# Optimization experiments

Measured on AMD Instinct MI355X. Metric: run time of the kernel, lower is better.

## Reference

```python
import jax, jax.numpy as jnp
import numpy as np
from jax import lax

B, D, H = 32768, 128, 256
N_ITER = 20


def setup_inputs() -> dict:
    key = jax.random.key(0)
    ks = jax.random.split(key, 7)
    return {
        "r": jax.random.normal(ks[0], (B, D), dtype=jnp.float32),
        "s": jax.random.normal(ks[1], (B, 1), dtype=jnp.float32),
        "pivot": jax.random.normal(ks[2], (D,), dtype=jnp.float32),
        "W1": jax.random.normal(ks[3], (D, H), dtype=jnp.float32) * 0.1,
        "b1": jax.random.normal(ks[4], (H,), dtype=jnp.float32) * 0.1,
        "w2": jax.random.normal(ks[5], (H,), dtype=jnp.float32) * 0.1,
        "b2": jax.random.normal(ks[6], (1,), dtype=jnp.float32) * 0.1,
        "n_iter": N_ITER,
    }


def _omega_step(x, W1, b1, w2, b2):
    # scalar implicit field omega evaluated on [B, D] points -> positive step in (0, 0.1)
    h = jnp.tanh(x @ W1 + b1)                      # [B, H]
    return 0.05 * (1.0 + jnp.tanh(h @ w2 + b2[0]))  # [B]


def reference(r, s, pivot, W1, b1, w2, b2, n_iter):
    # normalize ray directions; norm is detached in the original (stop_gradient)
    norm_of_x = jnp.linalg.norm(r, axis=1, keepdims=True)  # [B, 1]
    r_norm = r / lax.stop_gradient(norm_of_x)              # [B, D]

    # 20-step sphere-tracing-style ray marching along r_norm from pivot
    def step(alpha, _):
        x = pivot[None, :] + alpha[:, None] * r_norm       # [B, D]
        return alpha + _omega_step(x, W1, b1, w2, b2), None

    alpha0 = jnp.zeros((r.shape[0],), dtype=r.dtype)
    res_alpha, _ = lax.scan(step, alpha0, None, length=n_iter)  # [B]

    scale = jax.nn.sigmoid(s) * res_alpha[:, None]         # [B, 1]
    res_x = pivot[None, :] + scale * r_norm                # [B, D]
    return res_x
```

## Files before the change

kernel.cpp:

```cpp
#include <hip/hip_runtime.h>

#define DIM 128
#define HID 256
#define K2LE 2.885390081777927f
#define NTILES 16

typedef __attribute__((ext_vector_type(8))) short bf16x8;
typedef __attribute__((ext_vector_type(4))) float f32x4;

__device__ __forceinline__ unsigned short f2bf(float f) {
    union { float f; unsigned u; } x; x.f = f;
    unsigned r = x.u + 0x7fffu + ((x.u >> 16) & 1u);
    return (unsigned short)(r >> 16);
}
__device__ __forceinline__ float bflo(unsigned u) { return __uint_as_float(u << 16); }
__device__ __forceinline__ float bfhi(unsigned u) { return __uint_as_float(u & 0xffff0000u); }

__device__ __forceinline__ float sigmoid_fast(float x) {
    float t = __builtin_amdgcn_exp2f(-x * 1.4426950408889634f);
    return __builtin_amdgcn_rcpf(1.0f + t);
}

__device__ __forceinline__ float row16_allreduce(float x) {
    int t;
    t = __builtin_amdgcn_update_dpp(0, __float_as_int(x), 0xB1, 0xf, 0xf, true);
    x += __int_as_float(t);
    t = __builtin_amdgcn_update_dpp(0, __float_as_int(x), 0x4E, 0xf, 0xf, true);
    x += __int_as_float(t);
    t = __builtin_amdgcn_update_dpp(0, __float_as_int(x), 0x124, 0xf, 0xf, true);
    x += __int_as_float(t);
    t = __builtin_amdgcn_update_dpp(0, __float_as_int(x), 0x128, 0xf, 0xf, true);
    x += __int_as_float(t);
    return x;
}

__global__ void k_prep(const float* __restrict__ pivot,
                       const float* __restrict__ W1,
                       const float* __restrict__ b1,
                       const float* __restrict__ w2,
                       float* __restrict__ c2p,
                       float* __restrict__ w2p,
                       uint4* __restrict__ W1f) {
    const int tid = threadIdx.x;
    if (blockIdx.x == 0) {
        float a = b1[tid];
#pragma unroll 8
        for (int d = 0; d < DIM; ++d) a = fmaf(pivot[d], W1[d * HID + tid], a);
        const int pidx = (tid & 15) * 16 + (tid >> 4);
        c2p[pidx] = K2LE * a;
        w2p[pidx] = w2[tid];
    }
    const int e  = blockIdx.x * 256 + tid;
    const int m  = e & 15;
    const int q  = (e >> 4) & 3;
    const int kk = (e >> 6) & 3;
    const int nt = e >> 8;
    const int n  = nt * 16 + m;
    const int k0 = kk * 32 + q * 8;
    unsigned w[4];
#pragma unroll
    for (int p = 0; p < 4; ++p) {
        unsigned lo = f2bf(W1[(k0 + 2 * p    ) * HID + n] * K2LE);
        unsigned hi = f2bf(W1[(k0 + 2 * p + 1) * HID + n] * K2LE);
        w[p] = lo | (hi << 16);
    }
    W1f[e] = make_uint4(w[0], w[1], w[2], w[3]);
}

__global__ __launch_bounds__(256, 8) void k_main(
    const float* __restrict__ r,
    const float* __restrict__ s,
    const float* __restrict__ pivot,
    const float* __restrict__ c2p,
    const float* __restrict__ w2p,
    const float* __restrict__ b2,
    const int* __restrict__ n_iter_p,
    const uint4* __restrict__ W1f,
    float* __restrict__ out)
{
    __shared__ unsigned short rnbf[16][128];
    __shared__ float g_x[16][HID];

    const int tid   = threadIdx.x;
    const int lane  = tid & 63;
    const int wave  = tid >> 6;
    const int m     = lane & 15;
    const int q     = lane >> 4;
    const int ray_l = wave * 4 + q;
    const int ray_g = blockIdx.x * 16 + ray_l;
    const int n_iter = *n_iter_p;

    float4 v0 = *(const float4*)&r[ray_g * DIM + m * 8];
    float4 v1 = *(const float4*)&r[ray_g * DIM + m * 8 + 4];
    float ss = v0.x*v0.x + v0.y*v0.y + v0.z*v0.z + v0.w*v0.w
             + v1.x*v1.x + v1.y*v1.y + v1.z*v1.z + v1.w*v1.w;
    ss = row16_allreduce(ss);
    const float inv = __builtin_amdgcn_rsqf(ss);
    unsigned p0 = (unsigned)f2bf(v0.x*inv) | ((unsigned)f2bf(v0.y*inv) << 16);
    unsigned p1 = (unsigned)f2bf(v0.z*inv) | ((unsigned)f2bf(v0.w*inv) << 16);
    unsigned p2 = (unsigned)f2bf(v1.x*inv) | ((unsigned)f2bf(v1.y*inv) << 16);
    unsigned p3 = (unsigned)f2bf(v1.z*inv) | ((unsigned)f2bf(v1.w*inv) << 16);
    *(uint4*)&rnbf[ray_l][m * 8] = make_uint4(p0, p1, p2, p3);
    __syncthreads();

    bf16x8 afrag[4];
#pragma unroll
    for (int kk = 0; kk < 4; ++kk)
        afrag[kk] = *(const bf16x8*)&rnbf[m][kk * 32 + q * 8];

    const bf16x8* __restrict__ wf = (const bf16x8*)W1f;
    const int fb = q * 16 + m;
#pragma unroll
    for (int t = 0; t < 4; ++t) {
        const int nt = wave * 4 + t;
        f32x4 a = {0.f, 0.f, 0.f, 0.f};
#pragma unroll
        for (int kk = 0; kk < 4; ++kk)
            a = __builtin_amdgcn_mfma_f32_16x16x32_bf16(
                    afrag[kk], wf[nt * 256 + kk * 64 + fb], a, 0, 0, 0);
#pragma unroll
        for (int r4 = 0; r4 < 4; ++r4)
            g_x[q * 4 + r4][nt * 16 + m] = a[r4];
    }
    __syncthreads();

    float g[16], c[16], w[16];
#pragma unroll
    for (int i = 0; i < 16; ++i) g[i] = g_x[ray_l][i * 16 + m];
#pragma unroll
    for (int i = 0; i < 4; ++i) {
        float4 cv = *(const float4*)(c2p + m * 16 + i * 4);
        float4 wv = *(const float4*)(w2p + m * 16 + i * 4);
        c[4*i]=cv.x; c[4*i+1]=cv.y; c[4*i+2]=cv.z; c[4*i+3]=cv.w;
        w[4*i]=wv.x; w[4*i+1]=wv.y; w[4*i+2]=wv.z; w[4*i+3]=wv.w;
    }
    float S = 0.f;
#pragma unroll
    for (int i = 0; i < 16; ++i) S += w[i];
    S = row16_allreduce(S);
    const float C0 = K2LE * (S + b2[0]);

    float alpha = 0.f;
    for (int it = 0; it < n_iter; ++it) {
        float p = 0.f;
#pragma unroll
        for (int i = 0; i < 16; ++i) {
            float u = __builtin_amdgcn_rcpf(
                __builtin_amdgcn_exp2f(fmaf(alpha, g[i], c[i])) + 1.0f);
            p = fmaf(w[i], u, p);
        }
        p = row16_allreduce(p);
        float v = __builtin_amdgcn_rcpf(
            __builtin_amdgcn_exp2f(fmaf(-2.0f * K2LE, p, C0)) + 1.0f);
        alpha += fmaf(-0.1f, v, 0.1f);
    }

    const float sc = sigmoid_fast(s[ray_g]) * alpha;
    uint4 rl = *(const uint4*)&rnbf[ray_l][m * 8];
    float4 pv0 = *(const float4*)(pivot + m * 8);
    float4 pv1 = *(const float4*)(pivot + m * 8 + 4);
    float4 o0, o1;
    o0.x = fmaf(sc, bflo(rl.x), pv0.x);
    o0.y = fmaf(sc, bfhi(rl.x), pv0.y);
    o0.z = fmaf(sc, bflo(rl.y), pv0.z);
    o0.w = fmaf(sc, bfhi(rl.y), pv0.w);
    o1.x = fmaf(sc, bflo(rl.z), pv1.x);
    o1.y = fmaf(sc, bfhi(rl.z), pv1.y);
    o1.z = fmaf(sc, bflo(rl.w), pv1.z);
    o1.w = fmaf(sc, bfhi(rl.w), pv1.w);
    *(float4*)(out + ray_g * DIM + m * 8)     = o0;
    *(float4*)(out + ray_g * DIM + m * 8 + 4) = o1;
}

extern "C" void kernel_launch(void* const* d_in, const int* in_sizes, int n_in,
                              void* d_out, int out_size, void* d_ws, size_t ws_size,
                              hipStream_t stream) {
    const float* r      = (const float*)d_in[0];
    const float* s      = (const float*)d_in[1];
    const float* pivot  = (const float*)d_in[2];
    const float* W1     = (const float*)d_in[3];
    const float* b1     = (const float*)d_in[4];
    const float* w2     = (const float*)d_in[5];
    const float* b2     = (const float*)d_in[6];
    const int*   n_iter = (const int*)d_in[7];
    float* out = (float*)d_out;

    const int B = in_sizes[0] / DIM;

    char* ws = (char*)d_ws;
    float* c2p = (float*)(ws);
    float* w2p = (float*)(ws + 1024);
    uint4* W1f = (uint4*)(ws + 4096);

    k_prep<<<16, 256, 0, stream>>>(pivot, W1, b1, w2, c2p, w2p, W1f);
    k_main<<<B / 16, 256, 0, stream>>>(r, s, pivot, c2p, w2p, b2, n_iter,
                                       W1f, out);
}
```

Measured before the change: 123.4 us.

## Batch four reciprocals into one, pad LDS arrays, and hoist constant loads

The inner march loop now combines four sigmoid terms over a common denominator, so it issues one rcp per four hidden units instead of four, at the cost of extra multiplies. The shared-memory arrays are padded to reduce LDS bank conflicts, and the loads of c2p, w2p, s and b2 are moved before the MFMA phase so their latency overlaps it. Launch bounds drop from 8 to 6 waves per SIMD, which gives the compiler more registers. The common-denominator product of four (exp2+1) terms can overflow to inf when the exponents are large, which risks NaN or accuracy loss.

```diff
diff --git a/kernel.cpp b/kernel.cpp
--- a/kernel.cpp
+++ b/kernel.cpp
@@ -4,6 +4,8 @@
 #define HID 256
 #define K2LE 2.885390081777927f
 #define NTILES 16
+#define RNPAD 136
+#define GXPAD 260
 
 typedef __attribute__((ext_vector_type(8))) short bf16x8;
 typedef __attribute__((ext_vector_type(4))) float f32x4;
@@ -67,7 +69,7 @@
     W1f[e] = make_uint4(w[0], w[1], w[2], w[3]);
 }
 
-__global__ __launch_bounds__(256, 8) void k_main(
+__global__ __launch_bounds__(256, 6) void k_main(
     const float* __restrict__ r,
     const float* __restrict__ s,
     const float* __restrict__ pivot,
@@ -78,8 +80,8 @@
     const uint4* __restrict__ W1f,
     float* __restrict__ out)
 {
-    __shared__ unsigned short rnbf[16][128];
-    __shared__ float g_x[16][HID];
+    __shared__ unsigned short rnbf[16][RNPAD];
+    __shared__ float g_x[16][GXPAD];
 
     const int tid   = threadIdx.x;
     const int lane  = tid & 63;
@@ -92,6 +94,17 @@
 
     float4 v0 = *(const float4*)&r[ray_g * DIM + m * 8];
     float4 v1 = *(const float4*)&r[ray_g * DIM + m * 8 + 4];
+    const float sv  = s[ray_g];
+    float c[16], w[16];
+#pragma unroll
+    for (int i = 0; i < 4; ++i) {
+        float4 cv = *(const float4*)(c2p + m * 16 + i * 4);
+        float4 wv = *(const float4*)(w2p + m * 16 + i * 4);
+        c[4*i]=cv.x; c[4*i+1]=cv.y; c[4*i+2]=cv.z; c[4*i+3]=cv.w;
+        w[4*i]=wv.x; w[4*i+1]=wv.y; w[4*i+2]=wv.z; w[4*i+3]=wv.w;
+    }
+    const float b2v = b2[0];
+
     float ss = v0.x*v0.x + v0.y*v0.y + v0.z*v0.z + v0.w*v0.w
              + v1.x*v1.x + v1.y*v1.y + v1.z*v1.z + v1.w*v1.w;
     ss = row16_allreduce(ss);
@@ -122,32 +135,35 @@
         for (int r4 = 0; r4 < 4; ++r4)
             g_x[q * 4 + r4][nt * 16 + m] = a[r4];
     }
-    __syncthreads();
-
-    float g[16], c[16], w[16];
-#pragma unroll
-    for (int i = 0; i < 16; ++i) g[i] = g_x[ray_l][i * 16 + m];
-#pragma unroll
-    for (int i = 0; i < 4; ++i) {
-        float4 cv = *(const float4*)(c2p + m * 16 + i * 4);
-        float4 wv = *(const float4*)(w2p + m * 16 + i * 4);
-        c[4*i]=cv.x; c[4*i+1]=cv.y; c[4*i+2]=cv.z; c[4*i+3]=cv.w;
-        w[4*i]=wv.x; w[4*i+1]=wv.y; w[4*i+2]=wv.z; w[4*i+3]=wv.w;
-    }
+
     float S = 0.f;
 #pragma unroll
     for (int i = 0; i < 16; ++i) S += w[i];
     S = row16_allreduce(S);
-    const float C0 = K2LE * (S + b2[0]);
+    const float C0 = K2LE * (S + b2v);
+    __syncthreads();
+
+    float g[16];
+#pragma unroll
+    for (int i = 0; i < 16; ++i) g[i] = g_x[ray_l][i * 16 + m];
 
     float alpha = 0.f;
     for (int it = 0; it < n_iter; ++it) {
         float p = 0.f;
 #pragma unroll
-        for (int i = 0; i < 16; ++i) {
-            float u = __builtin_amdgcn_rcpf(
-                __builtin_amdgcn_exp2f(fmaf(alpha, g[i], c[i])) + 1.0f);
-            p = fmaf(w[i], u, p);
+        for (int qd = 0; qd < 4; ++qd) {
+            const int b = qd * 4;
+            float A0 = __builtin_amdgcn_exp2f(fmaf(alpha, g[b+0], c[b+0])) + 1.0f;
+            float A1 = __builtin_amdgcn_exp2f(fmaf(alpha, g[b+1], c[b+1])) + 1.0f;
+            float A2 = __builtin_amdgcn_exp2f(fmaf(alpha, g[b+2], c[b+2])) + 1.0f;
+            float A3 = __builtin_amdgcn_exp2f(fmaf(alpha, g[b+3], c[b+3])) + 1.0f;
+            float P01 = A0 * A1;
+            float P23 = A2 * A3;
+            float n01 = fmaf(w[b+0], A1, w[b+1] * A0);
+            float n23 = fmaf(w[b+2], A3, w[b+3] * A2);
+            float num = fmaf(n01, P23, n23 * P01);
+            float den = P01 * P23;
+            p = fmaf(num, __builtin_amdgcn_rcpf(den), p);
         }
         p = row16_allreduce(p);
         float v = __builtin_amdgcn_rcpf(
@@ -155,7 +171,7 @@
         alpha += fmaf(-0.1f, v, 0.1f);
     }
 
-    const float sc = sigmoid_fast(s[ray_g]) * alpha;
+    const float sc = sigmoid_fast(sv) * alpha;
     uint4 rl = *(const uint4*)&rnbf[ray_l][m * 8];
     float4 pv0 = *(const float4*)(pivot + m * 8);
     float4 pv1 = *(const float4*)(pivot + m * 8 + 4);
```

Result: no change. 122.5 us (-0.7%).
